# Kernel tuning notes

Hardware: AMD Instinct MI355X
Metric: run time of the kernel (lower is better)

Reference implementation:

```python
import jax, jax.numpy as jnp
import numpy as np
from jax import lax

DN = ('NCHW', 'OIHW', 'NCHW')

def _attn(x, w):
    # x: [B, C, H, W]; channel pool -> [B, 2, H, W]
    pool = jnp.concatenate([x.max(axis=1, keepdims=True), x.mean(axis=1, keepdims=True)], axis=1)
    g = lax.conv_general_dilated(pool, w, (1, 1), [(3, 3), (3, 3)], dimension_numbers=DN)
    return x * jax.nn.sigmoid(g)

def setup_inputs() -> dict:
    key = jax.random.key(0)
    k0, k1, k2, k3, k4 = jax.random.split(key, 5)
    B, C, H, W = 16, 128, 32, 512
    x = jax.random.normal(k0, (B, C, H, W), dtype=jnp.float32)
    wg = jax.random.normal(k1, (C, C // 2, 1, 3), dtype=jnp.float32) * 0.05  # groups=2 conv weight
    w1 = jax.random.normal(k2, (1, 2, 7, 7), dtype=jnp.float32) * 0.1
    w2 = jax.random.normal(k3, (1, 2, 7, 7), dtype=jnp.float32) * 0.1
    w3 = jax.random.normal(k4, (1, 2, 7, 7), dtype=jnp.float32) * 0.1
    return {"x": x, "wg": wg, "w1": w1, "w2": w2, "w3": w3}

def reference(x, wg, w1, w2, w3):
    # grouped (1,3) conv, padding (0,1), groups=2, no bias
    x = lax.conv_general_dilated(x, wg, (1, 1), [(0, 0), (1, 1)],
                                 dimension_numbers=DN, feature_group_count=2)
    o1 = _attn(x, w1)
    o2 = jnp.transpose(_attn(jnp.transpose(x, (0, 2, 1, 3)), w2), (0, 2, 1, 3))
    o3 = jnp.transpose(_attn(jnp.transpose(x, (0, 3, 2, 1)), w3), (0, 3, 2, 1))
    return (o1 + o2 + o3) / 3.0
```

## Files before the change

kernel.cpp:

```cpp
#include <hip/hip_runtime.h>
#include <math.h>

#define B 16
#define C 128
#define H 32
#define W 512

typedef short bf16x4 __attribute__((ext_vector_type(4)));
typedef short bf16x8 __attribute__((ext_vector_type(8)));
typedef float f32x4 __attribute__((ext_vector_type(4)));

static __device__ inline unsigned short f2bf(float f) {
    unsigned u = __builtin_bit_cast(unsigned, f);
    u += 0x7fffu + ((u >> 16) & 1u);
    return (unsigned short)(u >> 16);
}
static __device__ inline unsigned pack2(float a, float b) {
    unsigned u;
    asm("v_cvt_pk_bf16_f32 %0, %1, %2" : "=v"(u) : "v"(a), "v"(b));
    return u;
}
static __device__ inline float bflo(unsigned u) {
    return __builtin_bit_cast(float, u << 16);
}
static __device__ inline float bfhi(unsigned u) {
    return __builtin_bit_cast(float, u & 0xffff0000u);
}

__global__ __launch_bounds__(256) void prep_wT(const float* __restrict__ wg,
                                               unsigned short* __restrict__ wT) {
    const int e = blockIdx.x * 256 + threadIdx.x;
    if (e >= 24576) return;
    const int g   = e / 12288;
    const int rem = e - g * 12288;
    const int tap = rem >> 12;
    const int o   = (rem >> 6) & 63;
    const int ci  = rem & 63;
    wT[e] = f2bf(wg[((size_t)(g * 64 + o) * 64 + ci) * 3 + tap]);
}

__global__ __launch_bounds__(256) void conv_pools(
    const float* __restrict__ x, const unsigned short* __restrict__ wT,
    unsigned* __restrict__ pool3p, unsigned* __restrict__ pool1p,
    float* __restrict__ pool2) {
    __shared__ __align__(16) char xsb[2][34 * 144];
    __shared__ __align__(16) float ytile[2][32][68];

    const int bx = blockIdx.x;
    const int f  = bx & 31;
    const int g  = f & 1;
    const int b  = f >> 1;
    const int wq = bx >> 5;
    const int t  = threadIdx.x;
    const int lane = t & 63;
    const int col  = lane & 15;
    const int q    = lane >> 4;
    const int wave = t >> 6;

    const unsigned short* wA =
        wT + (size_t)g * 12288 + wave * 1024 + col * 64 + q * 8;
    bf16x8 wfr[3][2];
#pragma unroll
    for (int tap = 0; tap < 3; ++tap)
#pragma unroll
        for (int kk = 0; kk < 2; ++kk)
            wfr[tap][kk] = *(const bf16x8*)(wA + tap * 4096 + kk * 32);

    float a[2][4];
    float hv = 0.f;
    const int w0l = (t & 7) * 4;
    const int ci0 = (t >> 3) * 2;
    const float* xb0 = x + (size_t)(b * C + g * 64 + ci0) * (H * W) + wq * 32 + w0l;
    const int side = (t >> 6) & 1;
    const int hci  = t & 63;
    const int gw   = wq * 32 + (side ? 32 : -1);
    const bool hvalid = (t < 128) && (side ? (wq < 15) : (wq > 0));
    const float* xh0 = x + (size_t)(b * C + g * 64 + hci) * (H * W) + gw;

    auto LOADX = [&](int h) {
        const float4 v0 = *(const float4*)(xb0 + h * W);
        const float4 v1 = *(const float4*)(xb0 + (size_t)(H * W) + h * W);
        a[0][0] = v0.x; a[0][1] = v0.y; a[0][2] = v0.z; a[0][3] = v0.w;
        a[1][0] = v1.x; a[1][1] = v1.y; a[1][2] = v1.z; a[1][3] = v1.w;
        hv = hvalid ? xh0[h * W] : 0.f;
    };
    auto WRITEX = [&](char* buf) {
#pragma unroll
        for (int j = 0; j < 4; ++j)
            *(unsigned*)(buf + (size_t)(w0l + j + 1) * 144 + ci0 * 2) =
                pack2(a[0][j], a[1][j]);
        if (t < 128)
            *(unsigned short*)(buf + (size_t)(side ? 33 : 0) * 144 + hci * 2) = f2bf(hv);
    };

    f32x4 mH[2], sH[2];
#pragma unroll
    for (int wt = 0; wt < 2; ++wt) {
        mH[wt] = (f32x4){-INFINITY, -INFINITY, -INFINITY, -INFINITY};
        sH[wt] = (f32x4){0.f, 0.f, 0.f, 0.f};
    }

    const int wl = t >> 3;
    const int e  = t & 7;

    LOADX(0);
    WRITEX(xsb[0]);
    LOADX(1);
    __syncthreads();

    for (int h = 0; h < H; ++h) {
        const int cur = h & 1;

        f32x4 acc[2];
        acc[0] = (f32x4){0.f, 0.f, 0.f, 0.f};
        acc[1] = (f32x4){0.f, 0.f, 0.f, 0.f};
        {
            const char* ab = xsb[cur] + q * 16;
#pragma unroll
            for (int wt = 0; wt < 2; ++wt)
#pragma unroll
                for (int kk = 0; kk < 2; ++kk)
#pragma unroll
                    for (int tap = 0; tap < 3; ++tap) {
                        const bf16x8 xf = *(const bf16x8*)(
                            ab + (size_t)(wt * 16 + col + tap) * 144 + kk * 64);
                        acc[wt] = __builtin_amdgcn_mfma_f32_16x16x32_bf16(
                            xf, wfr[tap][kk], acc[wt], 0, 0, 0);
                    }
        }

#pragma unroll
        for (int wt = 0; wt < 2; ++wt)
#pragma unroll
            for (int r = 0; r < 4; ++r) {
                mH[wt][r] = fmaxf(mH[wt][r], acc[wt][r]);
                sH[wt][r] += acc[wt][r];
            }

        {
            float m = acc[0][0], s = acc[0][0];
            m = fmaxf(fmaxf(m, acc[0][1]), fmaxf(acc[0][2], acc[0][3]));
            s += acc[0][1] + acc[0][2] + acc[0][3];
#pragma unroll
            for (int r = 0; r < 4; ++r) {
                m = fmaxf(m, acc[1][r]);
                s += acc[1][r];
            }
            m = fmaxf(m, __shfl_xor(m, 16)); s += __shfl_xor(s, 16);
            m = fmaxf(m, __shfl_xor(m, 32)); s += __shfl_xor(s, 32);
            if (lane < 16)
                pool3p[((size_t)(wq * B + b) * H + h) * C + g * 64 + wave * 16 + lane] =
                    pack2(m, s);
        }

#pragma unroll
        for (int wt = 0; wt < 2; ++wt)
#pragma unroll
            for (int r = 0; r < 4; ++r)
                ytile[cur][wt * 16 + q * 4 + r][wave * 16 + col] = acc[wt][r];

        if (h < H - 1) WRITEX(xsb[cur ^ 1]);
        if (h < H - 2) LOADX(h + 2);
        __syncthreads();

        {
            const f32x4 v0 = *(const f32x4*)&ytile[cur][wl][e * 8];
            const f32x4 v1 = *(const f32x4*)&ytile[cur][wl][e * 8 + 4];
            float m = fmaxf(fmaxf(v0[0], v0[1]), fmaxf(v0[2], v0[3]));
            float s = v0[0] + v0[1] + v0[2] + v0[3];
            m = fmaxf(m, fmaxf(fmaxf(v1[0], v1[1]), fmaxf(v1[2], v1[3])));
            s += v1[0] + v1[1] + v1[2] + v1[3];
#pragma unroll
            for (int off = 1; off <= 4; off <<= 1) {
                m = fmaxf(m, __shfl_xor(m, off));
                s += __shfl_xor(s, off);
            }
            if (e == 0)
                pool1p[((size_t)(g * B + b) * H + h) * W + wq * 32 + wl] = pack2(m, s);
        }
    }

    {
        const int o = g * 64 + wave * 16 + col;
        float* p2m = pool2 + ((size_t)(b * 2 + 0) * C + o) * W + wq * 32 + q * 4;
        float* p2s = pool2 + ((size_t)(b * 2 + 1) * C + o) * W + wq * 32 + q * 4;
#pragma unroll
        for (int wt = 0; wt < 2; ++wt) {
            *(f32x4*)(p2m + wt * 16) = mH[wt];
            f32x4 sv = sH[wt];
            sv[0] *= (1.f / H); sv[1] *= (1.f / H);
            sv[2] *= (1.f / H); sv[3] *= (1.f / H);
            *(f32x4*)(p2s + wt * 16) = sv;
        }
    }
}

__global__ __launch_bounds__(256) void conv_apply(
    const float* __restrict__ x, const unsigned short* __restrict__ wT,
    const float* __restrict__ s1, const float* __restrict__ s2,
    const float* __restrict__ s3, float* __restrict__ out) {
    __shared__ __align__(16) char xsb[2][34 * 144];

    const int bx = blockIdx.x;
    const int f  = bx & 31;
    const int g  = f & 1;
    const int b  = f >> 1;
    const int chunk = bx >> 5;
    const int wq = chunk >> 2;
    const int hq = chunk & 3;
    const int h0 = hq * 8;
    const int t  = threadIdx.x;
    const int lane = t & 63;
    const int col  = lane & 15;
    const int q    = lane >> 4;
    const int wave = t >> 6;

    const unsigned short* wA =
        wT + (size_t)g * 12288 + wave * 1024 + col * 64 + q * 8;
    bf16x8 wfr[3][2];
#pragma unroll
    for (int tap = 0; tap < 3; ++tap)
#pragma unroll
        for (int kk = 0; kk < 2; ++kk)
            wfr[tap][kk] = *(const bf16x8*)(wA + tap * 4096 + kk * 32);

    float a[2][4];
    float hv = 0.f;
    const int w0l = (t & 7) * 4;
    const int ci0 = (t >> 3) * 2;
    const float* xb0 = x + (size_t)(b * C + g * 64 + ci0) * (H * W) + wq * 32 + w0l;
    const int side = (t >> 6) & 1;
    const int hci  = t & 63;
    const int gw   = wq * 32 + (side ? 32 : -1);
    const bool hvalid = (t < 128) && (side ? (wq < 15) : (wq > 0));
    const float* xh0 = x + (size_t)(b * C + g * 64 + hci) * (H * W) + gw;

    auto LOADX = [&](int h) {
        const float4 v0 = *(const float4*)(xb0 + h * W);
        const float4 v1 = *(const float4*)(xb0 + (size_t)(H * W) + h * W);
        a[0][0] = v0.x; a[0][1] = v0.y; a[0][2] = v0.z; a[0][3] = v0.w;
        a[1][0] = v1.x; a[1][1] = v1.y; a[1][2] = v1.z; a[1][3] = v1.w;
        hv = hvalid ? xh0[h * W] : 0.f;
    };
    auto WRITEX = [&](char* buf) {
#pragma unroll
        for (int j = 0; j < 4; ++j)
            *(unsigned*)(buf + (size_t)(w0l + j + 1) * 144 + ci0 * 2) =
                pack2(a[0][j], a[1][j]);
        if (t < 128)
            *(unsigned short*)(buf + (size_t)(side ? 33 : 0) * 144 + hci * 2) = f2bf(hv);
    };

    const int o = g * 64 + wave * 16 + col;
    const float4 g2a = *(const float4*)(s2 + ((size_t)b * C + o) * W + wq * 32 + q * 4);
    const float4 g2b = *(const float4*)(s2 + ((size_t)b * C + o) * W + wq * 32 + q * 4 + 16);

    LOADX(h0);
    WRITEX(xsb[0]);
    LOADX(h0 + 1);
    __syncthreads();

    for (int hh = 0; hh < 8; ++hh) {
        const int h   = h0 + hh;
        const int cur = hh & 1;

        f32x4 acc[2];
        acc[0] = (f32x4){0.f, 0.f, 0.f, 0.f};
        acc[1] = (f32x4){0.f, 0.f, 0.f, 0.f};
        {
            const char* ab = xsb[cur] + q * 16;
#pragma unroll
            for (int wt = 0; wt < 2; ++wt)
#pragma unroll
                for (int kk = 0; kk < 2; ++kk)
#pragma unroll
                    for (int tap = 0; tap < 3; ++tap) {
                        const bf16x8 xf = *(const bf16x8*)(
                            ab + (size_t)(wt * 16 + col + tap) * 144 + kk * 64);
                        acc[wt] = __builtin_amdgcn_mfma_f32_16x16x32_bf16(
                            xf, wfr[tap][kk], acc[wt], 0, 0, 0);
                    }
        }

        const float4 g1a = *(const float4*)(s1 + ((size_t)b * H + h) * W + wq * 32 + q * 4);
        const float4 g1b = *(const float4*)(s1 + ((size_t)b * H + h) * W + wq * 32 + q * 4 + 16);
        const float  g3v = s3[((size_t)b * H + h) * C + o];
        const float  k   = 1.f / 3.f;

        float* ob = out + ((size_t)(b * C + o) * H + h) * W + wq * 32 + q * 4;
        f32x4 o0, o1;
        o0[0] = acc[0][0] * (g1a.x + g2a.x + g3v) * k;
        o0[1] = acc[0][1] * (g1a.y + g2a.y + g3v) * k;
        o0[2] = acc[0][2] * (g1a.z + g2a.z + g3v) * k;
        o0[3] = acc[0][3] * (g1a.w + g2a.w + g3v) * k;
        o1[0] = acc[1][0] * (g1b.x + g2b.x + g3v) * k;
        o1[1] = acc[1][1] * (g1b.y + g2b.y + g3v) * k;
        o1[2] = acc[1][2] * (g1b.z + g2b.z + g3v) * k;
        o1[3] = acc[1][3] * (g1b.w + g2b.w + g3v) * k;
        *(f32x4*)ob        = o0;
        *(f32x4*)(ob + 16) = o1;

        if (hh < 7) WRITEX(xsb[cur ^ 1]);
        if (hh < 6) LOADX(h + 2);
        __syncthreads();
    }
}

__global__ __launch_bounds__(256) void combine(const unsigned* __restrict__ p1p,
                                               const unsigned* __restrict__ p3p,
                                               float* __restrict__ pool1,
                                               float* __restrict__ pool3) {
    const int bid = blockIdx.x;
    if (bid < 256) {
        const int n = bid * 256 + threadIdx.x;
        const int idx4 = n * 4;
        const uint4 u0 = *(const uint4*)(p1p + idx4);
        const uint4 u1 = *(const uint4*)(p1p + 262144 + idx4);
        const int b = idx4 >> 14;
        const int o = idx4 & 16383;
        float4 m, s;
        const float k = 1.f / C;
        m.x = fmaxf(bflo(u0.x), bflo(u1.x)); s.x = (bfhi(u0.x) + bfhi(u1.x)) * k;
        m.y = fmaxf(bflo(u0.y), bflo(u1.y)); s.y = (bfhi(u0.y) + bfhi(u1.y)) * k;
        m.z = fmaxf(bflo(u0.z), bflo(u1.z)); s.z = (bfhi(u0.z) + bfhi(u1.z)) * k;
        m.w = fmaxf(bflo(u0.w), bflo(u1.w)); s.w = (bfhi(u0.w) + bfhi(u1.w)) * k;
        *(float4*)(pool1 + ((size_t)(b * 2 + 0) * H * W) + o) = m;
        *(float4*)(pool1 + ((size_t)(b * 2 + 1) * H * W) + o) = s;
    } else {
        const int n = (bid - 256) * 256 + threadIdx.x;
        const int b = n >> 12;
        const int o = n & 4095;
        float m = -INFINITY, s = 0.f;
#pragma unroll
        for (int wq = 0; wq < 16; ++wq) {
            const unsigned u = p3p[(size_t)(wq * B + b) * 4096 + o];
            m = fmaxf(m, bflo(u));
            s += bfhi(u);
        }
        pool3[((size_t)(b * 2 + 0) * H * C) + o] = m;
        pool3[((size_t)(b * 2 + 1) * H * C) + o] = s * (1.f / W);
    }
}

__global__ __launch_bounds__(256) void gates(
    const float* __restrict__ pool1, const float* __restrict__ pool2,
    const float* __restrict__ pool3, const float* __restrict__ w1,
    const float* __restrict__ w2, const float* __restrict__ w3,
    float* __restrict__ s1, float* __restrict__ s2, float* __restrict__ s3) {
    const int bid = blockIdx.x;
    const float* pin; const float* wgt; float* so; int P, Q, n;
    if (bid < 256)       { pin = pool1; wgt = w1; so = s1; P = H; Q = W;
                           n = bid * 256 + threadIdx.x; }
    else if (bid < 1280) { pin = pool2; wgt = w2; so = s2; P = C; Q = W;
                           n = (bid - 256) * 256 + threadIdx.x; }
    else                 { pin = pool3; wgt = w3; so = s3; P = H; Q = C;
                           n = (bid - 1280) * 256 + threadIdx.x; }
    const int q4   = Q >> 2;
    const int q0   = (n % q4) * 4;
    const int rest = n / q4;
    const int p    = rest % P;
    const int b    = rest / P;
    float acc0 = 0.f, acc1 = 0.f, acc2 = 0.f, acc3 = 0.f;
#pragma unroll
    for (int c2 = 0; c2 < 2; ++c2) {
#pragma unroll
        for (int i = 0; i < 7; ++i) {
            const int pp = p + i - 3;
            if (pp < 0 || pp >= P) continue;
            const float* row = pin + ((size_t)(b * 2 + c2) * P + pp) * Q;
            float win[10];
#pragma unroll
            for (int j = 0; j < 10; ++j) {
                const int qq = q0 + j - 3;
                win[j] = (qq >= 0 && qq < Q) ? row[qq] : 0.f;
            }
            const float* wr = wgt + c2 * 49 + i * 7;
#pragma unroll
            for (int j = 0; j < 7; ++j) {
                const float wv = wr[j];
                acc0 += win[j]     * wv;
                acc1 += win[j + 1] * wv;
                acc2 += win[j + 2] * wv;
                acc3 += win[j + 3] * wv;
            }
        }
    }
    float4 o;
    o.x = 1.f / (1.f + expf(-acc0));
    o.y = 1.f / (1.f + expf(-acc1));
    o.z = 1.f / (1.f + expf(-acc2));
    o.w = 1.f / (1.f + expf(-acc3));
    *(float4*)(so + (size_t)n * 4) = o;
}

extern "C" void kernel_launch(void* const* d_in, const int* in_sizes, int n_in,
                              void* d_out, int out_size, void* d_ws, size_t ws_size,
                              hipStream_t stream) {
    const float* x  = (const float*)d_in[0];
    const float* wg = (const float*)d_in[1];
    const float* w1 = (const float*)d_in[2];
    const float* w2 = (const float*)d_in[3];
    const float* w3 = (const float*)d_in[4];
    float* out = (float*)d_out;
    float* ws  = (float*)d_ws;

    unsigned* pool1p = (unsigned*)ws;
    unsigned* pool3p = (unsigned*)(ws + 524288);
    float* pool2 = ws + 1572864;
    float* pool1 = ws + 3670016;
    float* pool3 = ws + 4194304;
    unsigned short* wT = (unsigned short*)(ws + 4325376);
    float* s1 = ws;
    float* s3 = ws + 262144;
    float* s2 = ws + 524288;

    prep_wT<<<dim3(96), 256, 0, stream>>>(wg, wT);
    conv_pools<<<dim3(512), 256, 0, stream>>>(x, wT, pool3p, pool1p, pool2);
    combine<<<dim3(512), 256, 0, stream>>>(pool1p, pool3p, pool1, pool3);
    gates<<<dim3(1344), 256, 0, stream>>>(pool1, pool2, pool3, w1, w2, w3, s1, s2, s3);
    conv_apply<<<dim3(2048), 256, 0, stream>>>(x, wT, s1, s2, s3, out);
}
```

Measured before the change: 156.9 us.

## Split conv_pools over H halves and store pool2 partials as packed bf16

Doubles the conv_pools grid by giving each block 16 of the 32 H rows instead of all of them. The idea is that 512 blocks underfill the GPU and add latency from long serial loops. Per-half H pool partials (max and sum) are packed into a single bf16x2 word and merged in place by a new branch in the combine kernel. The gates kernel gets a specialised path that reads the packed pool2 data. This halves the pool2 traffic but lowers the precision of those intermediates to bf16 and adds an extra combine pass.

After: 135.5 us. 1.16x faster.

```diff
diff --git a/kernel.cpp b/kernel.cpp
--- a/kernel.cpp
+++ b/kernel.cpp
@@ -42,7 +42,7 @@
 __global__ __launch_bounds__(256) void conv_pools(
     const float* __restrict__ x, const unsigned short* __restrict__ wT,
     unsigned* __restrict__ pool3p, unsigned* __restrict__ pool1p,
-    float* __restrict__ pool2) {
+    unsigned* __restrict__ pool2p) {
     __shared__ __align__(16) char xsb[2][34 * 144];
     __shared__ __align__(16) float ytile[2][32][68];
 
@@ -50,7 +50,10 @@
     const int f  = bx & 31;
     const int g  = f & 1;
     const int b  = f >> 1;
-    const int wq = bx >> 5;
+    const int chunk = bx >> 5;
+    const int wq = chunk >> 1;
+    const int hq = chunk & 1;
+    const int h0 = hq * 16;
     const int t  = threadIdx.x;
     const int lane = t & 63;
     const int col  = lane & 15;
@@ -103,13 +106,14 @@
     const int wl = t >> 3;
     const int e  = t & 7;
 
-    LOADX(0);
+    LOADX(h0);
     WRITEX(xsb[0]);
-    LOADX(1);
+    LOADX(h0 + 1);
     __syncthreads();
 
-    for (int h = 0; h < H; ++h) {
-        const int cur = h & 1;
+    for (int hh = 0; hh < 16; ++hh) {
+        const int h   = h0 + hh;
+        const int cur = hh & 1;
 
         f32x4 acc[2];
         acc[0] = (f32x4){0.f, 0.f, 0.f, 0.f};
@@ -159,8 +163,8 @@
             for (int r = 0; r < 4; ++r)
                 ytile[cur][wt * 16 + q * 4 + r][wave * 16 + col] = acc[wt][r];
 
-        if (h < H - 1) WRITEX(xsb[cur ^ 1]);
-        if (h < H - 2) LOADX(h + 2);
+        if (hh < 15) WRITEX(xsb[cur ^ 1]);
+        if (hh < 14) LOADX(h + 2);
         __syncthreads();
 
         {
@@ -182,15 +186,15 @@
 
     {
         const int o = g * 64 + wave * 16 + col;
-        float* p2m = pool2 + ((size_t)(b * 2 + 0) * C + o) * W + wq * 32 + q * 4;
-        float* p2s = pool2 + ((size_t)(b * 2 + 1) * C + o) * W + wq * 32 + q * 4;
+        unsigned* p2 = pool2p + ((size_t)(hq * B + b) * C + o) * W + wq * 32 + q * 4;
 #pragma unroll
         for (int wt = 0; wt < 2; ++wt) {
-            *(f32x4*)(p2m + wt * 16) = mH[wt];
-            f32x4 sv = sH[wt];
-            sv[0] *= (1.f / H); sv[1] *= (1.f / H);
-            sv[2] *= (1.f / H); sv[3] *= (1.f / H);
-            *(f32x4*)(p2s + wt * 16) = sv;
+            uint4 pk;
+            pk.x = pack2(mH[wt][0], sH[wt][0]);
+            pk.y = pack2(mH[wt][1], sH[wt][1]);
+            pk.z = pack2(mH[wt][2], sH[wt][2]);
+            pk.w = pack2(mH[wt][3], sH[wt][3]);
+            *(uint4*)(p2 + wt * 16) = pk;
         }
     }
 }
@@ -308,6 +312,7 @@
 
 __global__ __launch_bounds__(256) void combine(const unsigned* __restrict__ p1p,
                                                const unsigned* __restrict__ p3p,
+                                               unsigned* __restrict__ p2p,
                                                float* __restrict__ pool1,
                                                float* __restrict__ pool3) {
     const int bid = blockIdx.x;
@@ -326,7 +331,7 @@
         m.w = fmaxf(bflo(u0.w), bflo(u1.w)); s.w = (bfhi(u0.w) + bfhi(u1.w)) * k;
         *(float4*)(pool1 + ((size_t)(b * 2 + 0) * H * W) + o) = m;
         *(float4*)(pool1 + ((size_t)(b * 2 + 1) * H * W) + o) = s;
-    } else {
+    } else if (bid < 512) {
         const int n = (bid - 256) * 256 + threadIdx.x;
         const int b = n >> 12;
         const int o = n & 4095;
@@ -339,22 +344,68 @@
         }
         pool3[((size_t)(b * 2 + 0) * H * C) + o] = m;
         pool3[((size_t)(b * 2 + 1) * H * C) + o] = s * (1.f / W);
+    } else {
+        const int n = (bid - 512) * 256 + threadIdx.x;
+        const int idx4 = n * 4;
+        const uint4 u0 = *(const uint4*)(p2p + idx4);
+        const uint4 u1 = *(const uint4*)(p2p + 1048576 + idx4);
+        const float k = 1.f / H;
+        uint4 r;
+        r.x = pack2(fmaxf(bflo(u0.x), bflo(u1.x)), (bfhi(u0.x) + bfhi(u1.x)) * k);
+        r.y = pack2(fmaxf(bflo(u0.y), bflo(u1.y)), (bfhi(u0.y) + bfhi(u1.y)) * k);
+        r.z = pack2(fmaxf(bflo(u0.z), bflo(u1.z)), (bfhi(u0.z) + bfhi(u1.z)) * k);
+        r.w = pack2(fmaxf(bflo(u0.w), bflo(u1.w)), (bfhi(u0.w) + bfhi(u1.w)) * k);
+        *(uint4*)(p2p + idx4) = r;
     }
 }
 
 __global__ __launch_bounds__(256) void gates(
-    const float* __restrict__ pool1, const float* __restrict__ pool2,
+    const float* __restrict__ pool1, const unsigned* __restrict__ pool2,
     const float* __restrict__ pool3, const float* __restrict__ w1,
     const float* __restrict__ w2, const float* __restrict__ w3,
     float* __restrict__ s1, float* __restrict__ s2, float* __restrict__ s3) {
     const int bid = blockIdx.x;
+    if (bid >= 256 && bid < 1280) {
+        const int n  = (bid - 256) * 256 + threadIdx.x;
+        const int q0 = (n & 127) * 4;
+        const int p  = (n >> 7) & 127;
+        const int b  = n >> 14;
+        float acc0 = 0.f, acc1 = 0.f, acc2 = 0.f, acc3 = 0.f;
+#pragma unroll
+        for (int i = 0; i < 7; ++i) {
+            const int pp = p + i - 3;
+            if (pp < 0 || pp >= C) continue;
+            const unsigned* row = pool2 + ((size_t)b * C + pp) * W;
+            unsigned win[10];
+#pragma unroll
+            for (int j = 0; j < 10; ++j) {
+                const int qq = q0 + j - 3;
+                win[j] = (qq >= 0 && qq < W) ? row[qq] : 0u;
+            }
+            const float* wr0 = w2 + i * 7;
+            const float* wr1 = w2 + 49 + i * 7;
+#pragma unroll
+            for (int j = 0; j < 7; ++j) {
+                const float wv0 = wr0[j], wv1 = wr1[j];
+                acc0 += bflo(win[j])     * wv0 + bfhi(win[j])     * wv1;
+                acc1 += bflo(win[j + 1]) * wv0 + bfhi(win[j + 1]) * wv1;
+                acc2 += bflo(win[j + 2]) * wv0 + bfhi(win[j + 2]) * wv1;
+                acc3 += bflo(win[j + 3]) * wv0 + bfhi(win[j + 3]) * wv1;
+            }
+        }
+        float4 o;
+        o.x = 1.f / (1.f + expf(-acc0));
+        o.y = 1.f / (1.f + expf(-acc1));
+        o.z = 1.f / (1.f + expf(-acc2));
+        o.w = 1.f / (1.f + expf(-acc3));
+        *(float4*)(s2 + (size_t)n * 4) = o;
+        return;
+    }
     const float* pin; const float* wgt; float* so; int P, Q, n;
-    if (bid < 256)       { pin = pool1; wgt = w1; so = s1; P = H; Q = W;
-                           n = bid * 256 + threadIdx.x; }
-    else if (bid < 1280) { pin = pool2; wgt = w2; so = s2; P = C; Q = W;
-                           n = (bid - 256) * 256 + threadIdx.x; }
-    else                 { pin = pool3; wgt = w3; so = s3; P = H; Q = C;
-                           n = (bid - 1280) * 256 + threadIdx.x; }
+    if (bid < 256) { pin = pool1; wgt = w1; so = s1; P = H; Q = W;
+                     n = bid * 256 + threadIdx.x; }
+    else           { pin = pool3; wgt = w3; so = s3; P = H; Q = C;
+                     n = (bid - 1280) * 256 + threadIdx.x; }
     const int q4   = Q >> 2;
     const int q0   = (n % q4) * 4;
     const int rest = n / q4;
@@ -406,7 +457,7 @@
 
     unsigned* pool1p = (unsigned*)ws;
     unsigned* pool3p = (unsigned*)(ws + 524288);
-    float* pool2 = ws + 1572864;
+    unsigned* pool2p = (unsigned*)(ws + 1572864);
     float* pool1 = ws + 3670016;
     float* pool3 = ws + 4194304;
     unsigned short* wT = (unsigned short*)(ws + 4325376);
@@ -415,8 +466,8 @@
     float* s2 = ws + 524288;
 
     prep_wT<<<dim3(96), 256, 0, stream>>>(wg, wT);
-    conv_pools<<<dim3(512), 256, 0, stream>>>(x, wT, pool3p, pool1p, pool2);
-    combine<<<dim3(512), 256, 0, stream>>>(pool1p, pool3p, pool1, pool3);
-    gates<<<dim3(1344), 256, 0, stream>>>(pool1, pool2, pool3, w1, w2, w3, s1, s2, s3);
+    conv_pools<<<dim3(1024), 256, 0, stream>>>(x, wT, pool3p, pool1p, pool2p);
+    combine<<<dim3(1536), 256, 0, stream>>>(pool1p, pool3p, pool2p, pool1, pool3);
+    gates<<<dim3(1344), 256, 0, stream>>>(pool1, pool2p, pool3, w1, w2, w3, s1, s2, s3);
     conv_apply<<<dim3(2048), 256, 0, stream>>>(x, wT, s1, s2, s3, out);
 }
```
